# Optimization experiments

Hardware: AMD Instinct MI355X
Metric: run time of the kernel (lower is better)

Reference implementation:

```python
import jax, jax.numpy as jnp
import numpy as np
from jax import lax

MU = 0.1          # cfg MODEL.MU (FISTA step size)
LMBD = 0.1        # cfg MODEL.LAMBDA[0]
N_STEPS = 4       # cfg MODEL.NUM_LAYERS (unrolled FISTA iterations)
BN_EPS = 1e-5


def _norm_w(W):
    # DictBlock w_norm: each dictionary filter normalized to unit L2 norm.
    # torch does this under no_grad (in-place on .data), so the norm is a constant.
    n = jnp.sqrt(jnp.sum(W * W, axis=(1, 2, 3), keepdims=True))
    return W / lax.stop_gradient(n + 1e-12)


def _conv(x, W, stride, pad):
    return lax.conv_general_dilated(x, W, (stride, stride), [(pad, pad)] * 2,
                                    dimension_numbers=('NCHW', 'OIHW', 'NCHW'))


def _conv_t(z, W, stride, pad, out_pad):
    # torch conv_transpose2d(z, W, stride, padding=pad, output_padding=out_pad)
    k = W.shape[2]
    Wt = jnp.transpose(jnp.flip(W, (2, 3)), (1, 0, 2, 3))  # (in_ch, dict, k, k)
    p = k - 1 - pad
    return lax.conv_general_dilated(z, Wt, (1, 1), [(p, p + out_pad)] * 2,
                                    lhs_dilation=(stride, stride),
                                    dimension_numbers=('NCHW', 'OIHW', 'NCHW'))


def _shrink(c):
    # non-negative soft threshold: relu(c - lmbd*step)
    return jax.nn.relu(c - LMBD * MU)


def _dict_conv(x, W, stride):
    # Unrolled FISTA sparse coding: min_c 0.5||x - W^T c||^2 + lmbd||c||_1, c>=0
    W = _norm_w(W)
    out_pad = stride - 1
    c = _shrink(MU * _conv(x, W, stride, 1))
    c_pre = jnp.zeros_like(c)
    t = 1.0
    for _ in range(N_STEPS - 1):
        t_next = (1.0 + float(np.sqrt(1.0 + 4.0 * t * t))) / 2.0
        a = c + ((t - 1.0) / t_next) * (c - c_pre)
        c_pre = c
        r = x - _conv_t(a, W, stride, 1, out_pad)       # reconstruction residual
        c = _shrink(a + MU * _conv(r, W, stride, 1))    # proximal gradient step
        t = t_next
    return c


def _bn(x, g, b, m, v):
    # eval-mode BatchNorm2d with running stats
    scale = g * lax.rsqrt(v + BN_EPS)
    return (x - m[None, :, None, None]) * scale[None, :, None, None] + b[None, :, None, None]


def setup_inputs() -> dict:
    key = jax.random.key(0)
    ks = jax.random.split(key, 12)
    N, Cin, Cout, H = 32, 128, 256, 56
    x = jax.random.normal(ks[0], (N, Cin, H, H), jnp.float32)
    def unit_norm(W):
        return W / (jnp.sqrt(jnp.sum(W * W, axis=(1, 2, 3), keepdims=True)) + 1e-12)
    W1 = unit_norm(jax.random.normal(ks[1], (Cout, Cin, 3, 3), jnp.float32))
    W2 = unit_norm(jax.random.normal(ks[2], (Cout, Cout, 3, 3), jnp.float32))
    Wsc = jax.random.normal(ks[3], (Cout, Cin, 1, 1), jnp.float32) * 0.05
    def bn(k):
        k1, k2, k3, k4 = jax.random.split(k, 4)
        g = 1.0 + 0.1 * jax.random.normal(k1, (Cout,), jnp.float32)
        b = 0.1 * jax.random.normal(k2, (Cout,), jnp.float32)
        m = 0.1 * jax.random.normal(k3, (Cout,), jnp.float32)
        v = 0.5 + jax.random.uniform(k4, (Cout,), jnp.float32)
        return g, b, m, v
    bn1_g, bn1_b, bn1_m, bn1_v = bn(ks[4])
    bn2_g, bn2_b, bn2_m, bn2_v = bn(ks[5])
    bnsc_g, bnsc_b, bnsc_m, bnsc_v = bn(ks[6])
    return dict(x=x, W1=W1, W2=W2, Wsc=Wsc,
                bn1_g=bn1_g, bn1_b=bn1_b, bn1_m=bn1_m, bn1_v=bn1_v,
                bn2_g=bn2_g, bn2_b=bn2_b, bn2_m=bn2_m, bn2_v=bn2_v,
                bnsc_g=bnsc_g, bnsc_b=bnsc_b, bnsc_m=bnsc_m, bnsc_v=bnsc_v)


def reference(x, W1, W2, Wsc,
              bn1_g, bn1_b, bn1_m, bn1_v,
              bn2_g, bn2_b, bn2_m, bn2_v,
              bnsc_g, bnsc_b, bnsc_m, bnsc_v):
    out = _bn(_dict_conv(x, W1, 2), bn1_g, bn1_b, bn1_m, bn1_v)
    out = _bn(_dict_conv(out, W2, 1), bn2_g, bn2_b, bn2_m, bn2_v)
    sc = _bn(_conv(x, Wsc, 2, 0), bnsc_g, bnsc_b, bnsc_m, bnsc_v)
    return jax.nn.relu(out + sc)
```

## Files before the change

kernel.cpp:

```cpp
#include <hip/hip_runtime.h>
#include <math.h>

#define MU_F 0.1f
#define SHRINK_F 0.01f
#define BN_EPS_F 1e-5f

typedef _Float16 half_t;
typedef _Float16 half8 __attribute__((ext_vector_type(8)));
typedef float f32x4 __attribute__((ext_vector_type(4)));

#define LROW 40

template<int KS, int S, int PAD, int MODE>
__global__ __launch_bounds__(256, 2)
void conv_big(const half_t* __restrict__ Ag, const half_t* __restrict__ Xh,
              float* __restrict__ outF, half_t* __restrict__ outH,
              const half_t* __restrict__ auxH, const float* __restrict__ auxF,
              int CA, int Cout, int Hin, int Win, int Hout, int Wout, int ptiles,
              float alpha, float beta, float delta, int relu1,
              const float* __restrict__ pscale, const float* __restrict__ pbias,
              const float* __restrict__ aux3, int relu2)
{
    __shared__ __align__(16) half_t sm[256 * LROW];
    half_t* LA = sm;
    half_t* LB = sm + 128 * LROW;

    const int tid = threadIdx.x;
    const int wv = tid >> 6, ln = tid & 63;
    const int n = blockIdx.z;
    const int co0 = blockIdx.y * 128;
    const int wco = (wv & 1) * 64, wpx = (wv >> 1) * 64;

    int eh = 0, ew = 0, p0;
    if (MODE == 2) {
        int q = blockIdx.x / ptiles;
        p0 = (blockIdx.x - q * ptiles) * 128;
        eh = q >> 1; ew = q & 1;
    } else {
        p0 = blockIdx.x * 128;
    }

    const int Wd  = (MODE == 2) ? (Wout >> 1) : Wout;
    const int Hd  = (MODE == 2) ? (Hout >> 1) : Hout;
    const int PHW = Hd * Wd;
    const int K9  = KS * KS * CA;

    const int part = tid & 3;
    const int row0 = tid >> 2;

    size_t abase[2];
    abase[0] = (size_t)(co0 + row0) * K9 + part * 8;
    abase[1] = abase[0] + (size_t)64 * K9;

    int bph[2], bpw[2];
    bool bok0[2];
#pragma unroll
    for (int i = 0; i < 2; ++i) {
        int px = p0 + row0 + i * 64;
        bok0[i] = px < PHW;
        int ph = bok0[i] ? (px / Wd) : 0;
        bph[i] = ph; bpw[i] = px - ph * Wd;
    }

    f32x4 acc[4][4] = {};

    for (int kh = 0; kh < KS; ++kh)
    for (int kw = 0; kw < KS; ++kw) {
        if (MODE == 2) {
            if ((((kh ^ (eh + 1)) & 1) != 0) || (((kw ^ (ew + 1)) & 1) != 0)) continue;
        }
        const int tap = kh * KS + kw;
        size_t bb[2]; bool bvld[2];
#pragma unroll
        for (int i = 0; i < 2; ++i) {
            bool ok = bok0[i];
            int hh, ww2;
            if (MODE == 0) {
                hh = bph[i] * S - PAD + kh; ww2 = bpw[i] * S - PAD + kw;
                ok = ok && (unsigned)hh < (unsigned)Hin && (unsigned)ww2 < (unsigned)Win;
            } else if (MODE == 1) {
                hh = bph[i] + PAD - kh; ww2 = bpw[i] + PAD - kw;
                ok = ok && (unsigned)hh < (unsigned)Hin && (unsigned)ww2 < (unsigned)Win;
            } else {
                int nh = 2 * bph[i] + eh + PAD - kh, nw = 2 * bpw[i] + ew + PAD - kw;
                hh = nh >> 1; ww2 = nw >> 1;
                ok = ok && nh >= 0 && nw >= 0 && hh < Hin && ww2 < Win;
            }
            bvld[i] = ok;
            bb[i] = ok ? (((size_t)(n * Hin + hh) * Win + ww2) * CA + part * 8) : 0;
        }
        const size_t atap = (size_t)tap * CA;

        for (int c0 = 0; c0 < CA; c0 += 32) {
            half8 a0 = *(const half8*)(Ag + abase[0] + atap + c0);
            half8 a1 = *(const half8*)(Ag + abase[1] + atap + c0);
            half8 b0 = {}, b1 = {};
            if (bvld[0]) b0 = *(const half8*)(Xh + bb[0] + c0);
            if (bvld[1]) b1 = *(const half8*)(Xh + bb[1] + c0);
            *(half8*)(LA +  row0       * LROW + part * 8) = a0;
            *(half8*)(LA + (row0 + 64) * LROW + part * 8) = a1;
            *(half8*)(LB +  row0       * LROW + part * 8) = b0;
            *(half8*)(LB + (row0 + 64) * LROW + part * 8) = b1;
            __syncthreads();

            const int fr = ln & 15;
            const int koh = (ln >> 4) * 8;
            half8 fa[4], fb[4];
#pragma unroll
            for (int m = 0; m < 4; ++m)
                fa[m] = *(const half8*)(LA + (wco + m * 16 + fr) * LROW + koh);
#pragma unroll
            for (int t = 0; t < 4; ++t)
                fb[t] = *(const half8*)(LB + (wpx + t * 16 + fr) * LROW + koh);
#pragma unroll
            for (int m = 0; m < 4; ++m)
#pragma unroll
                for (int t = 0; t < 4; ++t)
                    acc[m][t] = __builtin_amdgcn_mfma_f32_16x16x32_f16(fa[m], fb[t], acc[m][t], 0, 0, 0);
            __syncthreads();
        }
    }

    const int fr = ln & 15;
    const int rg = ln >> 4;
#pragma unroll
    for (int t = 0; t < 4; ++t) {
        int px = p0 + wpx + t * 16 + fr;
        if (px >= PHW) continue;
        int ph = px / Wd, pw = px - ph * Wd;
        int oh, ow;
        if (MODE == 2) { oh = 2 * ph + eh; ow = 2 * pw + ew; }
        else           { oh = ph;          ow = pw; }
        size_t ghwc = ((size_t)(n * Hout + oh) * Wout + ow) * Cout;
#pragma unroll
        for (int m = 0; m < 4; ++m) {
#pragma unroll
            for (int r = 0; r < 4; ++r) {
                int co_l = co0 + wco + m * 16 + rg * 4 + r;
                size_t fidx = ((size_t)(n * Cout + co_l) * Hout + oh) * Wout + ow;
                float v = alpha * acc[m][t][r] + delta;
                if (auxH) v += beta * (float)auxH[ghwc + co_l];
                if (auxF) v += beta * auxF[fidx];
                if (relu1) v = fmaxf(v, 0.f);
                if (pscale) v = pscale[co_l] * v + pbias[co_l];
                if (aux3) v += aux3[fidx];
                if (relu2) v = fmaxf(v, 0.f);
                if (outH) outH[ghwc + co_l] = (half_t)v;
                else      outF[fidx] = v;
            }
        }
    }
}

template<int KT>
__global__ __launch_bounds__(256)
void pack_w(const float* __restrict__ W, half_t* __restrict__ Wh,
            half_t* __restrict__ WTh, int Cin, int Cout, int do_norm)
{
    __shared__ float red[256];
    int co = blockIdx.x, tid = threadIdx.x;
    int CK = Cin * KT;
    const float* w = W + (size_t)co * CK;
    float inv = 1.f;
    if (do_norm) {
        float s = 0.f;
        for (int i = tid; i < CK; i += 256) { float v = w[i]; s += v * v; }
        red[tid] = s; __syncthreads();
        for (int o = 128; o > 0; o >>= 1) {
            if (tid < o) red[tid] += red[tid + o];
            __syncthreads();
        }
        inv = 1.f / (sqrtf(red[0]) + 1e-12f);
    }
    for (int i = tid; i < CK; i += 256) {
        int ci = i / KT, tap = i - ci * KT;
        half_t h = (half_t)(w[i] * inv);
        Wh[((size_t)co * KT + tap) * Cin + ci] = h;
        if (WTh) WTh[((size_t)ci * KT + tap) * Cout + co] = h;
    }
}

__global__ __launch_bounds__(256)
void tx_kernel(const float* __restrict__ x, half_t* __restrict__ xTh)
{
    __shared__ __align__(16) half_t tl[56 * 136];
    int h = blockIdx.x, n = blockIdx.y, tid = threadIdx.x;
    for (int it = 0; it < 28; ++it) {
        int id = tid + it * 256;
        int c = id / 56, w0 = id - c * 56;
        tl[w0 * 136 + c] = (half_t)x[(((size_t)n * 128 + c) * 56 + h) * 56 + w0];
    }
    __syncthreads();
    if (tid < 224) {
        int w0 = tid >> 2, part = tid & 3;
        size_t base = (((size_t)n * 56 + h) * 56 + w0) * 128 + part * 32;
#pragma unroll
        for (int j = 0; j < 4; ++j)
            *(half8*)(xTh + base + j * 8) = *(const half8*)(tl + w0 * 136 + part * 32 + j * 8);
    }
}

__global__ __launch_bounds__(256)
void comb_kernel(const half_t* __restrict__ c, const half_t* __restrict__ p,
                 half_t* __restrict__ a, float w1, float w2, int n8)
{
    int i = blockIdx.x * 256 + threadIdx.x;
    if (i >= n8) return;
    half8 cv = ((const half8*)c)[i];
    half8 pv = ((const half8*)p)[i];
    half8 r;
#pragma unroll
    for (int j = 0; j < 8; ++j) r[j] = (half_t)(w1 * (float)cv[j] + w2 * (float)pv[j]);
    ((half8*)a)[i] = r;
}

__global__ __launch_bounds__(256)
void bn_prep_kernel(const float* __restrict__ g, const float* __restrict__ b,
                    const float* __restrict__ m, const float* __restrict__ v,
                    float* __restrict__ s, float* __restrict__ t, int C)
{
    int i = blockIdx.x * 256 + threadIdx.x;
    if (i < C) {
        float sc = g[i] * rsqrtf(v[i] + BN_EPS_F);
        s[i] = sc; t[i] = b[i] - m[i] * sc;
    }
}

extern "C" void kernel_launch(void* const* d_in, const int* in_sizes, int n_in,
                              void* d_out, int out_size, void* d_ws, size_t ws_size,
                              hipStream_t stream)
{
    (void)in_sizes; (void)n_in; (void)out_size;
    const float* x    = (const float*)d_in[0];
    const float* W1   = (const float*)d_in[1];
    const float* W2   = (const float*)d_in[2];
    const float* Wsc  = (const float*)d_in[3];
    const float* bn1g = (const float*)d_in[4];
    const float* bn1b = (const float*)d_in[5];
    const float* bn1m = (const float*)d_in[6];
    const float* bn1v = (const float*)d_in[7];
    const float* bn2g = (const float*)d_in[8];
    const float* bn2b = (const float*)d_in[9];
    const float* bn2m = (const float*)d_in[10];
    const float* bn2v = (const float*)d_in[11];
    const float* bscg = (const float*)d_in[12];
    const float* bscb = (const float*)d_in[13];
    const float* bscm = (const float*)d_in[14];
    const float* bscv = (const float*)d_in[15];

    const size_t NB = (size_t)32 * 256 * 28 * 28;
    const size_t NX = (size_t)32 * 128 * 56 * 56;

    char* base = (char*)d_ws;
    size_t off = 0;
    auto alloc = [&](size_t nbytes) -> void* {
        void* r = base + off;
        off = (off + nbytes + 255) & ~(size_t)255;
        return r;
    };
    half_t* Wh1  = (half_t*)alloc(294912 * 2);
    half_t* WTh1 = (half_t*)alloc(294912 * 2);
    half_t* Wh2  = (half_t*)alloc(589824 * 2);
    half_t* WTh2 = (half_t*)alloc(589824 * 2);
    half_t* Wsch = (half_t*)alloc(32768 * 2);
    float* bn1s = (float*)alloc(256 * 4);  float* bn1t = (float*)alloc(256 * 4);
    float* bn2s = (float*)alloc(256 * 4);  float* bn2t = (float*)alloc(256 * 4);
    float* bscs = (float*)alloc(256 * 4);  float* bsct = (float*)alloc(256 * 4);
    half_t* xTh  = (half_t*)alloc(NX * 2);
    half_t* r56h = xTh;
    half_t* Pa   = (half_t*)alloc(NB * 2);
    half_t* Pb   = (half_t*)alloc(NB * 2);
    half_t* Pc   = (half_t*)alloc(NB * 2);
    half_t* Py   = (half_t*)alloc(NB * 2);
    half_t* r28h = (half_t*)alloc(NB * 2);
    float*  scF  = (float*)alloc(NB * 4);
    if (off > ws_size) return;

    float* outp = (float*)d_out;

    double t = 1.0; float al[3];
    for (int i = 0; i < 3; ++i) {
        double tn = (1.0 + sqrt(1.0 + 4.0 * t * t)) / 2.0;
        al[i] = (float)((t - 1.0) / tn); t = tn;
    }

    const dim3 blk(256);
    const dim3 gF(7, 2, 32);
    const dim3 gT2(28, 1, 32);
    const int n8 = (int)(NB / 8);
    const dim3 gC((n8 + 255) / 256);
    const float* NF = nullptr;
    const half_t* NH = nullptr;
    float* NFo = nullptr;
    half_t* NHo = nullptr;

    pack_w<9><<<256, blk, 0, stream>>>(W1, Wh1, WTh1, 128, 256, 1);
    pack_w<9><<<256, blk, 0, stream>>>(W2, Wh2, WTh2, 256, 256, 1);
    pack_w<1><<<256, blk, 0, stream>>>(Wsc, Wsch, nullptr, 128, 256, 0);
    bn_prep_kernel<<<1, blk, 0, stream>>>(bn1g, bn1b, bn1m, bn1v, bn1s, bn1t, 256);
    bn_prep_kernel<<<1, blk, 0, stream>>>(bn2g, bn2b, bn2m, bn2v, bn2s, bn2t, 256);
    bn_prep_kernel<<<1, blk, 0, stream>>>(bscg, bscb, bscm, bscv, bscs, bsct, 256);
    tx_kernel<<<dim3(56, 32), blk, 0, stream>>>(x, xTh);

    conv_big<3,2,1,0><<<gF, blk, 0, stream>>>(Wh1, xTh, NFo, Pa, NH, NF,
        128, 256, 56, 56, 28, 28, 7, MU_F, 0.f, -SHRINK_F, 1, NF, NF, NF, 0);
    conv_big<1,2,0,0><<<gF, blk, 0, stream>>>(Wsch, xTh, scF, NHo, NH, NF,
        128, 256, 56, 56, 28, 28, 7, 1.f, 0.f, 0.f, 0, bscs, bsct, NF, 0);

    conv_big<3,2,1,2><<<gT2, blk, 0, stream>>>(WTh1, Pa, NFo, r56h, NH, x,
        256, 128, 28, 28, 56, 56, 7, -1.f, 1.f, 0.f, 0, NF, NF, NF, 0);
    conv_big<3,2,1,0><<<gF, blk, 0, stream>>>(Wh1, r56h, NFo, Pb, Pa, NF,
        128, 256, 56, 56, 28, 28, 7, MU_F, 1.f, -SHRINK_F, 1, NF, NF, NF, 0);

    comb_kernel<<<gC, blk, 0, stream>>>(Pb, Pa, Pc, 1.f + al[1], -al[1], n8);
    conv_big<3,2,1,2><<<gT2, blk, 0, stream>>>(WTh1, Pc, NFo, r56h, NH, x,
        256, 128, 28, 28, 56, 56, 7, -1.f, 1.f, 0.f, 0, NF, NF, NF, 0);
    conv_big<3,2,1,0><<<gF, blk, 0, stream>>>(Wh1, r56h, NFo, Pa, Pc, NF,
        128, 256, 56, 56, 28, 28, 7, MU_F, 1.f, -SHRINK_F, 1, NF, NF, NF, 0);

    comb_kernel<<<gC, blk, 0, stream>>>(Pa, Pb, Pc, 1.f + al[2], -al[2], n8);
    conv_big<3,2,1,2><<<gT2, blk, 0, stream>>>(WTh1, Pc, NFo, r56h, NH, x,
        256, 128, 28, 28, 56, 56, 7, -1.f, 1.f, 0.f, 0, NF, NF, NF, 0);
    conv_big<3,2,1,0><<<gF, blk, 0, stream>>>(Wh1, r56h, NFo, Py, Pc, NF,
        128, 256, 56, 56, 28, 28, 7, MU_F, 1.f, -SHRINK_F, 1, bn1s, bn1t, NF, 0);

    conv_big<3,1,1,0><<<gF, blk, 0, stream>>>(Wh2, Py, NFo, Pa, NH, NF,
        256, 256, 28, 28, 28, 28, 7, MU_F, 0.f, -SHRINK_F, 1, NF, NF, NF, 0);

    conv_big<3,1,1,1><<<gF, blk, 0, stream>>>(WTh2, Pa, NFo, r28h, Py, NF,
        256, 256, 28, 28, 28, 28, 7, -1.f, 1.f, 0.f, 0, NF, NF, NF, 0);
    conv_big<3,1,1,0><<<gF, blk, 0, stream>>>(Wh2, r28h, NFo, Pb, Pa, NF,
        256, 256, 28, 28, 28, 28, 7, MU_F, 1.f, -SHRINK_F, 1, NF, NF, NF, 0);

    comb_kernel<<<gC, blk, 0, stream>>>(Pb, Pa, Pc, 1.f + al[1], -al[1], n8);
    conv_big<3,1,1,1><<<gF, blk, 0, stream>>>(WTh2, Pc, NFo, r28h, Py, NF,
        256, 256, 28, 28, 28, 28, 7, -1.f, 1.f, 0.f, 0, NF, NF, NF, 0);
    conv_big<3,1,1,0><<<gF, blk, 0, stream>>>(Wh2, r28h, NFo, Pa, Pc, NF,
        256, 256, 28, 28, 28, 28, 7, MU_F, 1.f, -SHRINK_F, 1, NF, NF, NF, 0);

    comb_kernel<<<gC, blk, 0, stream>>>(Pa, Pb, Pc, 1.f + al[2], -al[2], n8);
    conv_big<3,1,1,1><<<gF, blk, 0, stream>>>(WTh2, Pc, NFo, r28h, Py, NF,
        256, 256, 28, 28, 28, 28, 7, -1.f, 1.f, 0.f, 0, NF, NF, NF, 0);
    conv_big<3,1,1,0><<<gF, blk, 0, stream>>>(Wh2, r28h, outp, NHo, Pc, NF,
        256, 256, 28, 28, 28, 28, 7, MU_F, 1.f, -SHRINK_F, 1, bn2s, bn2t, scF, 1);
}
```

Baseline: 1.330 ms.

## Double-buffer LDS tiles and prefetch next K-chunk into registers in conv GEMM

Flattens the tap×channel-chunk loops into a single loop and double-buffers the shared-memory tiles, so the global loads for step k+2 are in flight while MFMAs run on step k. This removes one of the two barriers per iteration and hides global-load latency behind compute. In exchange it doubles LDS use (40 KB per block), which may limit occupancy at two blocks per CU, and it assumes CA/32 is 4 or 8 (power-of-two channel-chunk count).

```diff
diff --git a/kernel.cpp b/kernel.cpp
--- a/kernel.cpp
+++ b/kernel.cpp
@@ -21,9 +21,7 @@
               const float* __restrict__ pscale, const float* __restrict__ pbias,
               const float* __restrict__ aux3, int relu2)
 {
-    __shared__ __align__(16) half_t sm[256 * LROW];
-    half_t* LA = sm;
-    half_t* LB = sm + 128 * LROW;
+    __shared__ __align__(16) half_t sm[2 * 256 * LROW];
 
     const int tid = threadIdx.x;
     const int wv = tid >> 6, ln = tid & 63;
@@ -48,12 +46,10 @@
     const int part = tid & 3;
     const int row0 = tid >> 2;
 
-    size_t abase[2];
-    abase[0] = (size_t)(co0 + row0) * K9 + part * 8;
-    abase[1] = abase[0] + (size_t)64 * K9;
-
-    int bph[2], bpw[2];
-    bool bok0[2];
+    const size_t abase0 = (size_t)(co0 + row0) * K9 + part * 8;
+    const size_t abase1 = abase0 + (size_t)64 * K9;
+
+    int bph[2], bpw[2]; bool bok0[2];
 #pragma unroll
     for (int i = 0; i < 2; ++i) {
         int px = p0 + row0 + i * 64;
@@ -62,19 +58,35 @@
         bph[i] = ph; bpw[i] = px - ph * Wd;
     }
 
-    f32x4 acc[4][4] = {};
-
-    for (int kh = 0; kh < KS; ++kh)
-    for (int kw = 0; kw < KS; ++kw) {
+    const int cpt = CA >> 5;
+    const int lgc = (cpt == 8) ? 3 : 2;
+    int ntap, lgj = 0, phh = 0, pww = 0;
+    if (MODE == 2) {
+        phh = (eh + 1) & 1; pww = (ew + 1) & 1;
+        lgj = ew;
+        ntap = (1 + eh) * (1 + ew);
+    } else {
+        ntap = KS * KS;
+    }
+    const int total = ntap << lgc;
+
+    auto fetch = [&](int flat, half8& a0, half8& a1, half8& b0, half8& b1) {
+        const int ci = flat & (cpt - 1);
+        const int ti = flat >> lgc;
+        int kh, kw;
         if (MODE == 2) {
-            if ((((kh ^ (eh + 1)) & 1) != 0) || (((kw ^ (ew + 1)) & 1) != 0)) continue;
-        }
-        const int tap = kh * KS + kw;
-        size_t bb[2]; bool bvld[2];
+            int i2 = ti >> lgj, j = ti & ((1 << lgj) - 1);
+            kh = phh + 2 * i2; kw = pww + 2 * j;
+        } else if (KS == 3) {
+            kh = (ti * 11) >> 5; kw = ti - 3 * kh;
+        } else { kh = 0; kw = 0; }
+        const int c0 = ci << 5;
+        const size_t aoff = (size_t)(kh * KS + kw) * CA + c0;
+        a0 = *(const half8*)(Ag + abase0 + aoff);
+        a1 = *(const half8*)(Ag + abase1 + aoff);
 #pragma unroll
         for (int i = 0; i < 2; ++i) {
-            bool ok = bok0[i];
-            int hh, ww2;
+            bool ok = bok0[i]; int hh, ww2;
             if (MODE == 0) {
                 hh = bph[i] * S - PAD + kh; ww2 = bpw[i] * S - PAD + kw;
                 ok = ok && (unsigned)hh < (unsigned)Hin && (unsigned)ww2 < (unsigned)Win;
@@ -86,42 +98,52 @@
                 hh = nh >> 1; ww2 = nw >> 1;
                 ok = ok && nh >= 0 && nw >= 0 && hh < Hin && ww2 < Win;
             }
-            bvld[i] = ok;
-            bb[i] = ok ? (((size_t)(n * Hin + hh) * Win + ww2) * CA + part * 8) : 0;
+            half8 v = {};
+            if (ok) v = *(const half8*)(Xh + ((size_t)(n * Hin + hh) * Win + ww2) * CA + c0 + part * 8);
+            if (i == 0) b0 = v; else b1 = v;
         }
-        const size_t atap = (size_t)tap * CA;
-
-        for (int c0 = 0; c0 < CA; c0 += 32) {
-            half8 a0 = *(const half8*)(Ag + abase[0] + atap + c0);
-            half8 a1 = *(const half8*)(Ag + abase[1] + atap + c0);
-            half8 b0 = {}, b1 = {};
-            if (bvld[0]) b0 = *(const half8*)(Xh + bb[0] + c0);
-            if (bvld[1]) b1 = *(const half8*)(Xh + bb[1] + c0);
-            *(half8*)(LA +  row0       * LROW + part * 8) = a0;
-            *(half8*)(LA + (row0 + 64) * LROW + part * 8) = a1;
-            *(half8*)(LB +  row0       * LROW + part * 8) = b0;
-            *(half8*)(LB + (row0 + 64) * LROW + part * 8) = b1;
-            __syncthreads();
-
-            const int fr = ln & 15;
-            const int koh = (ln >> 4) * 8;
-            half8 fa[4], fb[4];
-#pragma unroll
-            for (int m = 0; m < 4; ++m)
-                fa[m] = *(const half8*)(LA + (wco + m * 16 + fr) * LROW + koh);
-#pragma unroll
-            for (int t = 0; t < 4; ++t)
-                fb[t] = *(const half8*)(LB + (wpx + t * 16 + fr) * LROW + koh);
-#pragma unroll
-            for (int m = 0; m < 4; ++m)
-#pragma unroll
-                for (int t = 0; t < 4; ++t)
-                    acc[m][t] = __builtin_amdgcn_mfma_f32_16x16x32_f16(fa[m], fb[t], acc[m][t], 0, 0, 0);
+    };
+
+    f32x4 acc[4][4] = {};
+    half8 pa0, pa1, pb0, pb1;
+
+    fetch(0, pa0, pa1, pb0, pb1);
+    {
+        half_t* buf = sm;
+        *(half8*)(buf +  row0        * LROW + part * 8) = pa0;
+        *(half8*)(buf + (row0 +  64) * LROW + part * 8) = pa1;
+        *(half8*)(buf + (row0 + 128) * LROW + part * 8) = pb0;
+        *(half8*)(buf + (row0 + 192) * LROW + part * 8) = pb1;
+    }
+    if (total > 1) fetch(1, pa0, pa1, pb0, pb1);
+    __syncthreads();
+
+    const int fr = ln & 15, koh = (ln >> 4) * 8;
+    for (int k = 0; k < total; ++k) {
+        half_t* buf = sm + (k & 1) * (256 * LROW);
+        half8 fa[4], fb[4];
+#pragma unroll
+        for (int m = 0; m < 4; ++m)
+            fa[m] = *(const half8*)(buf + (wco + m * 16 + fr) * LROW + koh);
+#pragma unroll
+        for (int t2 = 0; t2 < 4; ++t2)
+            fb[t2] = *(const half8*)(buf + (128 + wpx + t2 * 16 + fr) * LROW + koh);
+#pragma unroll
+        for (int m = 0; m < 4; ++m)
+#pragma unroll
+            for (int t2 = 0; t2 < 4; ++t2)
+                acc[m][t2] = __builtin_amdgcn_mfma_f32_16x16x32_f16(fa[m], fb[t2], acc[m][t2], 0, 0, 0);
+        if (k + 1 < total) {
+            half_t* nb = sm + ((k + 1) & 1) * (256 * LROW);
+            *(half8*)(nb +  row0        * LROW + part * 8) = pa0;
+            *(half8*)(nb + (row0 +  64) * LROW + part * 8) = pa1;
+            *(half8*)(nb + (row0 + 128) * LROW + part * 8) = pb0;
+            *(half8*)(nb + (row0 + 192) * LROW + part * 8) = pb1;
+            if (k + 2 < total) fetch(k + 2, pa0, pa1, pb0, pb1);
             __syncthreads();
         }
     }
 
-    const int fr = ln & 15;
     const int rg = ln >> 4;
 #pragma unroll
     for (int t = 0; t < 4; ++t) {
```

Result: faster. 1.196 ms (-10.1%).

## Replace LDS-staged conv GEMM with register-direct MFMA fragment loads

Applied to the files above, without the earlier changes.

Drops LDS staging and barriers from the implicit-GEMM convolution. Weights are pre-packed into an MFMA-fragment layout, and each wave loads its A and B fragments straight from global memory into registers. Pixel tiles now span the batch dimension to cover 25088 positions, out-of-bounds taps read a zeroed page instead of branching, and epilogue loads and stores are vectorized. Residuals now go to their own buffer, and the shortcut is stored as fp16 rather than fp32. The trade is losing data reuse across waves through shared memory, so more global and L2 traffic, plus unrolled loops that may raise register pressure.

```diff
diff --git a/kernel.cpp b/kernel.cpp
--- a/kernel.cpp
+++ b/kernel.cpp
@@ -7,146 +7,133 @@
 
 typedef _Float16 half_t;
 typedef _Float16 half8 __attribute__((ext_vector_type(8)));
+typedef _Float16 half4 __attribute__((ext_vector_type(4)));
 typedef float f32x4 __attribute__((ext_vector_type(4)));
 
-#define LROW 40
-
-template<int KS, int S, int PAD, int MODE>
-__global__ __launch_bounds__(256, 2)
-void conv_big(const half_t* __restrict__ Ag, const half_t* __restrict__ Xh,
+template<int KS, int S, int PAD, int MODE, int CAT>
+__global__ __launch_bounds__(256)
+void conv_reg(const half_t* __restrict__ Af, const half_t* __restrict__ Xh,
               float* __restrict__ outF, half_t* __restrict__ outH,
-              const half_t* __restrict__ auxH, const float* __restrict__ auxF,
-              int CA, int Cout, int Hin, int Win, int Hout, int Wout, int ptiles,
-              float alpha, float beta, float delta, int relu1,
+              const half_t* __restrict__ auxH, const half_t* __restrict__ aux3H,
               const float* __restrict__ pscale, const float* __restrict__ pbias,
-              const float* __restrict__ aux3, int relu2)
-{
-    __shared__ __align__(16) half_t sm[256 * LROW];
-    half_t* LA = sm;
-    half_t* LB = sm + 128 * LROW;
-
+              const half_t* __restrict__ zpage,
+              int Cout, int Hin, int Win, int Hout, int Wout, int KT, int ptiles,
+              float alpha, float beta, float delta, int relu1, int relu2)
+{
     const int tid = threadIdx.x;
     const int wv = tid >> 6, ln = tid & 63;
-    const int n = blockIdx.z;
-    const int co0 = blockIdx.y * 128;
-    const int wco = (wv & 1) * 64, wpx = (wv >> 1) * 64;
-
-    int eh = 0, ew = 0, p0;
-    if (MODE == 2) {
-        int q = blockIdx.x / ptiles;
-        p0 = (blockIdx.x - q * ptiles) * 128;
-        eh = q >> 1; ew = q & 1;
-    } else {
-        p0 = blockIdx.x * 128;
-    }
-
-    const int Wd  = (MODE == 2) ? (Wout >> 1) : Wout;
-    const int Hd  = (MODE == 2) ? (Hout >> 1) : Hout;
-    const int PHW = Hd * Wd;
-    const int K9  = KS * KS * CA;
-
-    const int part = tid & 3;
-    const int row0 = tid >> 2;
-
-    size_t abase[2];
-    abase[0] = (size_t)(co0 + row0) * K9 + part * 8;
-    abase[1] = abase[0] + (size_t)64 * K9;
-
-    int bph[2], bpw[2];
-    bool bok0[2];
-#pragma unroll
-    for (int i = 0; i < 2; ++i) {
-        int px = p0 + row0 + i * 64;
-        bok0[i] = px < PHW;
-        int ph = bok0[i] ? (px / Wd) : 0;
-        bph[i] = ph; bpw[i] = px - ph * Wd;
-    }
-
+    const int g  = blockIdx.y * 2 + (wv & 1);
+    const int fr = ln & 15, rg = ln >> 4, ko8 = rg * 8;
+    const int PXTOT = 25088;
+
+    int eh = 0, ew = 0, bx = blockIdx.x;
+    if (MODE == 2) { int q = bx / ptiles; bx -= q * ptiles; eh = q >> 1; ew = q & 1; }
+    const int p0 = bx * 128 + (wv >> 1) * 64;
+
+    const int Wd   = (MODE == 2) ? (Wout >> 1) : Wout;
+    const int Hd   = (MODE == 2) ? (Hout >> 1) : Hout;
+    const int PHWI = Hd * Wd;
+
+    int phv[4], pwv[4], nv[4];
+    unsigned vb[4];
+#pragma unroll
+    for (int t = 0; t < 4; ++t) {
+        int px = p0 + t * 16 + fr;
+        int n  = px / PHWI; int rem = px - n * PHWI;
+        int ph = rem / Wd;  int pw  = rem - ph * Wd;
+        nv[t] = n; phv[t] = ph; pwv[t] = pw;
+        int ih0 = (MODE == 0) ? ph * S : ph;
+        int iw0 = (MODE == 0) ? pw * S : pw;
+        vb[t] = ((unsigned)(n * Hin + ih0) * Win + iw0) * CAT + ko8;
+    }
+
+    const half_t* Ap = Af + ((size_t)g * KT) * 2048 + ln * 8;
     f32x4 acc[4][4] = {};
-
+    constexpr int cpt = CAT / 32;
+
+#pragma unroll
     for (int kh = 0; kh < KS; ++kh)
+#pragma unroll
     for (int kw = 0; kw < KS; ++kw) {
-        if (MODE == 2) {
+        int dh, dw;
+        if (MODE == 0)      { dh = kh - PAD; dw = kw - PAD; }
+        else if (MODE == 1) { dh = PAD - kh; dw = PAD - kw; }
+        else {
             if ((((kh ^ (eh + 1)) & 1) != 0) || (((kw ^ (ew + 1)) & 1) != 0)) continue;
+            dh = (eh + PAD - kh) >> 1; dw = (ew + PAD - kw) >> 1;
+        }
+        const int off = (dh * Win + dw) * CAT;
+        const half_t* bp[4];
+#pragma unroll
+        for (int t = 0; t < 4; ++t) {
+            int ih = ((MODE == 0) ? phv[t] * S : phv[t]) + dh;
+            int iw = ((MODE == 0) ? pwv[t] * S : pwv[t]) + dw;
+            bool ok = (unsigned)ih < (unsigned)Hin && (unsigned)iw < (unsigned)Win;
+            bp[t] = ok ? (Xh + vb[t] + off) : zpage;
         }
         const int tap = kh * KS + kw;
-        size_t bb[2]; bool bvld[2];
-#pragma unroll
-        for (int i = 0; i < 2; ++i) {
-            bool ok = bok0[i];
-            int hh, ww2;
-            if (MODE == 0) {
-                hh = bph[i] * S - PAD + kh; ww2 = bpw[i] * S - PAD + kw;
-                ok = ok && (unsigned)hh < (unsigned)Hin && (unsigned)ww2 < (unsigned)Win;
-            } else if (MODE == 1) {
-                hh = bph[i] + PAD - kh; ww2 = bpw[i] + PAD - kw;
-                ok = ok && (unsigned)hh < (unsigned)Hin && (unsigned)ww2 < (unsigned)Win;
-            } else {
-                int nh = 2 * bph[i] + eh + PAD - kh, nw = 2 * bpw[i] + ew + PAD - kw;
-                hh = nh >> 1; ww2 = nw >> 1;
-                ok = ok && nh >= 0 && nw >= 0 && hh < Hin && ww2 < Win;
-            }
-            bvld[i] = ok;
-            bb[i] = ok ? (((size_t)(n * Hin + hh) * Win + ww2) * CA + part * 8) : 0;
-        }
-        const size_t atap = (size_t)tap * CA;
-
-        for (int c0 = 0; c0 < CA; c0 += 32) {
-            half8 a0 = *(const half8*)(Ag + abase[0] + atap + c0);
-            half8 a1 = *(const half8*)(Ag + abase[1] + atap + c0);
-            half8 b0 = {}, b1 = {};
-            if (bvld[0]) b0 = *(const half8*)(Xh + bb[0] + c0);
-            if (bvld[1]) b1 = *(const half8*)(Xh + bb[1] + c0);
-            *(half8*)(LA +  row0       * LROW + part * 8) = a0;
-            *(half8*)(LA + (row0 + 64) * LROW + part * 8) = a1;
-            *(half8*)(LB +  row0       * LROW + part * 8) = b0;
-            *(half8*)(LB + (row0 + 64) * LROW + part * 8) = b1;
-            __syncthreads();
-
-            const int fr = ln & 15;
-            const int koh = (ln >> 4) * 8;
+        const half_t* Apt = Ap + (size_t)(tap * cpt) * 2048;
+#pragma unroll
+        for (int ci = 0; ci < cpt; ++ci) {
             half8 fa[4], fb[4];
 #pragma unroll
             for (int m = 0; m < 4; ++m)
-                fa[m] = *(const half8*)(LA + (wco + m * 16 + fr) * LROW + koh);
+                fa[m] = *(const half8*)(Apt + ci * 2048 + m * 512);
 #pragma unroll
             for (int t = 0; t < 4; ++t)
-                fb[t] = *(const half8*)(LB + (wpx + t * 16 + fr) * LROW + koh);
+                fb[t] = *(const half8*)(bp[t] + ci * 32);
 #pragma unroll
             for (int m = 0; m < 4; ++m)
 #pragma unroll
                 for (int t = 0; t < 4; ++t)
                     acc[m][t] = __builtin_amdgcn_mfma_f32_16x16x32_f16(fa[m], fb[t], acc[m][t], 0, 0, 0);
-            __syncthreads();
-        }
-    }
-
-    const int fr = ln & 15;
-    const int rg = ln >> 4;
+        }
+    }
+
 #pragma unroll
     for (int t = 0; t < 4; ++t) {
-        int px = p0 + wpx + t * 16 + fr;
-        if (px >= PHW) continue;
-        int ph = px / Wd, pw = px - ph * Wd;
         int oh, ow;
-        if (MODE == 2) { oh = 2 * ph + eh; ow = 2 * pw + ew; }
-        else           { oh = ph;          ow = pw; }
-        size_t ghwc = ((size_t)(n * Hout + oh) * Wout + ow) * Cout;
+        if (MODE == 2) { oh = 2 * phv[t] + eh; ow = 2 * pwv[t] + ew; }
+        else           { oh = phv[t];          ow = pwv[t]; }
+        size_t gb = ((size_t)(nv[t] * Hout + oh) * Wout + ow) * Cout + g * 64;
 #pragma unroll
         for (int m = 0; m < 4; ++m) {
-#pragma unroll
-            for (int r = 0; r < 4; ++r) {
-                int co_l = co0 + wco + m * 16 + rg * 4 + r;
-                size_t fidx = ((size_t)(n * Cout + co_l) * Hout + oh) * Wout + ow;
-                float v = alpha * acc[m][t][r] + delta;
-                if (auxH) v += beta * (float)auxH[ghwc + co_l];
-                if (auxF) v += beta * auxF[fidx];
-                if (relu1) v = fmaxf(v, 0.f);
-                if (pscale) v = pscale[co_l] * v + pbias[co_l];
-                if (aux3) v += aux3[fidx];
-                if (relu2) v = fmaxf(v, 0.f);
-                if (outH) outH[ghwc + co_l] = (half_t)v;
-                else      outF[fidx] = v;
+            const int cb = m * 16 + rg * 4;
+            float v[4];
+#pragma unroll
+            for (int r = 0; r < 4; ++r) v[r] = alpha * acc[m][t][r] + delta;
+            if (auxH) {
+                half4 a1 = *(const half4*)(auxH + gb + cb);
+#pragma unroll
+                for (int r = 0; r < 4; ++r) v[r] += beta * (float)a1[r];
+            }
+            if (relu1)
+#pragma unroll
+                for (int r = 0; r < 4; ++r) v[r] = fmaxf(v[r], 0.f);
+            if (pscale) {
+                f32x4 s = *(const f32x4*)(pscale + g * 64 + cb);
+                f32x4 b = *(const f32x4*)(pbias  + g * 64 + cb);
+#pragma unroll
+                for (int r = 0; r < 4; ++r) v[r] = s[r] * v[r] + b[r];
+            }
+            if (aux3H) {
+                half4 a3 = *(const half4*)(aux3H + gb + cb);
+#pragma unroll
+                for (int r = 0; r < 4; ++r) v[r] += (float)a3[r];
+            }
+            if (relu2)
+#pragma unroll
+                for (int r = 0; r < 4; ++r) v[r] = fmaxf(v[r], 0.f);
+            if (outH) {
+                half4 o;
+#pragma unroll
+                for (int r = 0; r < 4; ++r) o[r] = (half_t)v[r];
+                *(half4*)(outH + gb + cb) = o;
+            } else {
+                const int co = g * 64 + cb;
+#pragma unroll
+                for (int r = 0; r < 4; ++r)
+                    outF[((size_t)(nv[t] * Cout + co + r) * Hout + oh) * Wout + ow] = v[r];
             }
         }
     }
@@ -181,6 +168,20 @@
 }
 
 __global__ __launch_bounds__(256)
+void pack_frag(const half_t* __restrict__ Wflat, half_t* __restrict__ Af,
+               int KT, int total8)
+{
+    int idx = blockIdx.x * 256 + threadIdx.x;
+    if (idx >= total8) return;
+    int l = idx & 63, m = (idx >> 6) & 3, t2 = idx >> 8;
+    int kc = t2 % KT, gg = t2 / KT;
+    int row = gg * 64 + m * 16 + (l & 15);
+    int koff = kc * 32 + (l >> 4) * 8;
+    int K9 = KT * 32;
+    *(half8*)(Af + (size_t)idx * 8) = *(const half8*)(Wflat + (size_t)row * K9 + koff);
+}
+
+__global__ __launch_bounds__(256)
 void tx_kernel(const float* __restrict__ x, half_t* __restrict__ xTh)
 {
     __shared__ __align__(16) half_t tl[56 * 136];
@@ -224,6 +225,13 @@
         float sc = g[i] * rsqrtf(v[i] + BN_EPS_F);
         s[i] = sc; t[i] = b[i] - m[i] * sc;
     }
+}
+
+__global__ __launch_bounds__(256)
+void zero_kernel(half_t* __restrict__ p, int n)
+{
+    int i = blockIdx.x * 256 + threadIdx.x;
+    if (i < n) p[i] = (half_t)0.f;
 }
 
 extern "C" void kernel_launch(void* const* d_in, const int* in_sizes, int n_in,
@@ -263,17 +271,23 @@
     half_t* Wh2  = (half_t*)alloc(589824 * 2);
     half_t* WTh2 = (half_t*)alloc(589824 * 2);
     half_t* Wsch = (half_t*)alloc(32768 * 2);
+    half_t* Af1  = (half_t*)alloc(294912 * 2);
+    half_t* AfT1 = (half_t*)alloc(294912 * 2);
+    half_t* Af2  = (half_t*)alloc(589824 * 2);
+    half_t* AfT2 = (half_t*)alloc(589824 * 2);
+    half_t* Afsc = (half_t*)alloc(32768 * 2);
     float* bn1s = (float*)alloc(256 * 4);  float* bn1t = (float*)alloc(256 * 4);
     float* bn2s = (float*)alloc(256 * 4);  float* bn2t = (float*)alloc(256 * 4);
     float* bscs = (float*)alloc(256 * 4);  float* bsct = (float*)alloc(256 * 4);
+    half_t* zp   = (half_t*)alloc(512 * 2);
     half_t* xTh  = (half_t*)alloc(NX * 2);
-    half_t* r56h = xTh;
+    half_t* r56h = (half_t*)alloc(NX * 2);
     half_t* Pa   = (half_t*)alloc(NB * 2);
     half_t* Pb   = (half_t*)alloc(NB * 2);
     half_t* Pc   = (half_t*)alloc(NB * 2);
     half_t* Py   = (half_t*)alloc(NB * 2);
     half_t* r28h = (half_t*)alloc(NB * 2);
-    float*  scF  = (float*)alloc(NB * 4);
+    half_t* Psc  = (half_t*)alloc(NB * 2);
     if (off > ws_size) return;
 
     float* outp = (float*)d_out;
@@ -285,8 +299,8 @@
     }
 
     const dim3 blk(256);
-    const dim3 gF(7, 2, 32);
-    const dim3 gT2(28, 1, 32);
+    const dim3 gF(196, 2);
+    const dim3 gT2(784, 1);
     const int n8 = (int)(NB / 8);
     const dim3 gC((n8 + 255) / 256);
     const float* NF = nullptr;
@@ -297,50 +311,56 @@
     pack_w<9><<<256, blk, 0, stream>>>(W1, Wh1, WTh1, 128, 256, 1);
     pack_w<9><<<256, blk, 0, stream>>>(W2, Wh2, WTh2, 256, 256, 1);
     pack_w<1><<<256, blk, 0, stream>>>(Wsc, Wsch, nullptr, 128, 256, 0);
+    pack_frag<<<(36864 + 255) / 256, blk, 0, stream>>>(Wh1,  Af1,  36, 36864);
+    pack_frag<<<(36864 + 255) / 256, blk, 0, stream>>>(WTh1, AfT1, 72, 36864);
+    pack_frag<<<(73728 + 255) / 256, blk, 0, stream>>>(Wh2,  Af2,  72, 73728);
+    pack_frag<<<(73728 + 255) / 256, blk, 0, stream>>>(WTh2, AfT2, 72, 73728);
+    pack_frag<<<(4096  + 255) / 256, blk, 0, stream>>>(Wsch, Afsc,  4, 4096);
     bn_prep_kernel<<<1, blk, 0, stream>>>(bn1g, bn1b, bn1m, bn1v, bn1s, bn1t, 256);
     bn_prep_kernel<<<1, blk, 0, stream>>>(bn2g, bn2b, bn2m, bn2v, bn2s, bn2t, 256);
     bn_prep_kernel<<<1, blk, 0, stream>>>(bscg, bscb, bscm, bscv, bscs, bsct, 256);
+    zero_kernel<<<2, blk, 0, stream>>>(zp, 512);
     tx_kernel<<<dim3(56, 32), blk, 0, stream>>>(x, xTh);
 
-    conv_big<3,2,1,0><<<gF, blk, 0, stream>>>(Wh1, xTh, NFo, Pa, NH, NF,
-        128, 256, 56, 56, 28, 28, 7, MU_F, 0.f, -SHRINK_F, 1, NF, NF, NF, 0);
-    conv_big<1,2,0,0><<<gF, blk, 0, stream>>>(Wsch, xTh, scF, NHo, NH, NF,
-        128, 256, 56, 56, 28, 28, 7, 1.f, 0.f, 0.f, 0, bscs, bsct, NF, 0);
-
-    conv_big<3,2,1,2><<<gT2, blk, 0, stream>>>(WTh1, Pa, NFo, r56h, NH, x,
-        256, 128, 28, 28, 56, 56, 7, -1.f, 1.f, 0.f, 0, NF, NF, NF, 0);
-    conv_big<3,2,1,0><<<gF, blk, 0, stream>>>(Wh1, r56h, NFo, Pb, Pa, NF,
-        128, 256, 56, 56, 28, 28, 7, MU_F, 1.f, -SHRINK_F, 1, NF, NF, NF, 0);
+    conv_reg<3,2,1,0,128><<<gF, blk, 0, stream>>>(Af1, xTh, NFo, Pa, NH, NH, NF, NF, zp,
+        256, 56, 56, 28, 28, 36, 196, MU_F, 0.f, -SHRINK_F, 1, 0);
+    conv_reg<1,2,0,0,128><<<gF, blk, 0, stream>>>(Afsc, xTh, NFo, Psc, NH, NH, bscs, bsct, zp,
+        256, 56, 56, 28, 28, 4, 196, 1.f, 0.f, 0.f, 0, 0);
+
+    conv_reg<3,2,1,2,256><<<gT2, blk, 0, stream>>>(AfT1, Pa, NFo, r56h, xTh, NH, NF, NF, zp,
+        128, 28, 28, 56, 56, 72, 196, -1.f, 1.f, 0.f, 0, 0);
+    conv_reg<3,2,1,0,128><<<gF, blk, 0, stream>>>(Af1, r56h, NFo, Pb, Pa, NH, NF, NF, zp,
+        256, 56, 56, 28, 28, 36, 196, MU_F, 1.f, -SHRINK_F, 1, 0);
 
     comb_kernel<<<gC, blk, 0, stream>>>(Pb, Pa, Pc, 1.f + al[1], -al[1], n8);
-    conv_big<3,2,1,2><<<gT2, blk, 0, stream>>>(WTh1, Pc, NFo, r56h, NH, x,
-        256, 128, 28, 28, 56, 56, 7, -1.f, 1.f, 0.f, 0, NF, NF, NF, 0);
-    conv_big<3,2,1,0><<<gF, blk, 0, stream>>>(Wh1, r56h, NFo, Pa, Pc, NF,
-        128, 256, 56, 56, 28, 28, 7, MU_F, 1.f, -SHRINK_F, 1, NF, NF, NF, 0);
+    conv_reg<3,2,1,2,256><<<gT2, blk, 0, stream>>>(AfT1, Pc, NFo, r56h, xTh, NH, NF, NF, zp,
+        128, 28, 28, 56, 56, 72, 196, -1.f, 1.f, 0.f, 0, 0);
+    conv_reg<3,2,1,0,128><<<gF, blk, 0, stream>>>(Af1, r56h, NFo, Pa, Pc, NH, NF, NF, zp,
+        256, 56, 56, 28, 28, 36, 196, MU_F, 1.f, -SHRINK_F, 1, 0);
 
     comb_kernel<<<gC, blk, 0, stream>>>(Pa, Pb, Pc, 1.f + al[2], -al[2], n8);
-    conv_big<3,2,1,2><<<gT2, blk, 0, stream>>>(WTh1, Pc, NFo, r56h, NH, x,
-        256, 128, 28, 28, 56, 56, 7, -1.f, 1.f, 0.f, 0, NF, NF, NF, 0);
-    conv_big<3,2,1,0><<<gF, blk, 0, stream>>>(Wh1, r56h, NFo, Py, Pc, NF,
-        128, 256, 56, 56, 28, 28, 7, MU_F, 1.f, -SHRINK_F, 1, bn1s, bn1t, NF, 0);
-
-    conv_big<3,1,1,0><<<gF, blk, 0, stream>>>(Wh2, Py, NFo, Pa, NH, NF,
-        256, 256, 28, 28, 28, 28, 7, MU_F, 0.f, -SHRINK_F, 1, NF, NF, NF, 0);
-
-    conv_big<3,1,1,1><<<gF, blk, 0, stream>>>(WTh2, Pa, NFo, r28h, Py, NF,
-        256, 256, 28, 28, 28, 28, 7, -1.f, 1.f, 0.f, 0, NF, NF, NF, 0);
-    conv_big<3,1,1,0><<<gF, blk, 0, stream>>>(Wh2, r28h, NFo, Pb, Pa, NF,
-        256, 256, 28, 28, 28, 28, 7, MU_F, 1.f, -SHRINK_F, 1, NF, NF, NF, 0);
+    conv_reg<3,2,1,2,256><<<gT2, blk, 0, stream>>>(AfT1, Pc, NFo, r56h, xTh, NH, NF, NF, zp,
+        128, 28, 28, 56, 56, 72, 196, -1.f, 1.f, 0.f, 0, 0);
+    conv_reg<3,2,1,0,128><<<gF, blk, 0, stream>>>(Af1, r56h, NFo, Py, Pc, NH, bn1s, bn1t, zp,
+        256, 56, 56, 28, 28, 36, 196, MU_F, 1.f, -SHRINK_F, 1, 0);
+
+    conv_reg<3,1,1,0,256><<<gF, blk, 0, stream>>>(Af2, Py, NFo, Pa, NH, NH, NF, NF, zp,
+        256, 28, 28, 28, 28, 72, 196, MU_F, 0.f, -SHRINK_F, 1, 0);
+
+    conv_reg<3,1,1,1,256><<<gF, blk, 0, stream>>>(AfT2, Pa, NFo, r28h, Py, NH, NF, NF, zp,
+        256, 28, 28, 28, 28, 72, 196, -1.f, 1.f, 0.f, 0, 0);
+    conv_reg<3,1,1,0,256><<<gF, blk, 0, stream>>>(Af2, r28h, NFo, Pb, Pa, NH, NF, NF, zp,
+        256, 28, 28, 28, 28, 72, 196, MU_F, 1.f, -SHRINK_F, 1, 0);
 
     comb_kernel<<<gC, blk, 0, stream>>>(Pb, Pa, Pc, 1.f + al[1], -al[1], n8);
-    conv_big<3,1,1,1><<<gF, blk, 0, stream>>>(WTh2, Pc, NFo, r28h, Py, NF,
-        256, 256, 28, 28, 28, 28, 7, -1.f, 1.f, 0.f, 0, NF, NF, NF, 0);
-    conv_big<3,1,1,0><<<gF, blk, 0, stream>>>(Wh2, r28h, NFo, Pa, Pc, NF,
-        256, 256, 28, 28, 28, 28, 7, MU_F, 1.f, -SHRINK_F, 1, NF, NF, NF, 0);
+    conv_reg<3,1,1,1,256><<<gF, blk, 0, stream>>>(AfT2, Pc, NFo, r28h, Py, NH, NF, NF, zp,
+        256, 28, 28, 28, 28, 72, 196, -1.f, 1.f, 0.f, 0, 0);
+    conv_reg<3,1,1,0,256><<<gF, blk, 0, stream>>>(Af2, r28h, NFo, Pa, Pc, NH, NF, NF, zp,
+        256, 28, 28, 28, 28, 72, 196, MU_F, 1.f, -SHRINK_F, 1, 0);
 
     comb_kernel<<<gC, blk, 0, stream>>>(Pa, Pb, Pc, 1.f + al[2], -al[2], n8);
-    conv_big<3,1,1,1><<<gF, blk, 0, stream>>>(WTh2, Pc, NFo, r28h, Py, NF,
-        256, 256, 28, 28, 28, 28, 7, -1.f, 1.f, 0.f, 0, NF, NF, NF, 0);
-    conv_big<3,1,1,0><<<gF, blk, 0, stream>>>(Wh2, r28h, outp, NHo, Pc, NF,
-        256, 256, 28, 28, 28, 28, 7, MU_F, 1.f, -SHRINK_F, 1, bn2s, bn2t, scF, 1);
-}
+    conv_reg<3,1,1,1,256><<<gF, blk, 0, stream>>>(AfT2, Pc, NFo, r28h, Py, NH, NF, NF, zp,
+        256, 28, 28, 28, 28, 72, 196, -1.f, 1.f, 0.f, 0, 0);
+    conv_reg<3,1,1,0,256><<<gF, blk, 0, stream>>>(Af2, r28h, outp, NHo, Pc, Psc, bn2s, bn2t, zp,
+        256, 28, 28, 28, 28, 72, 196, MU_F, 1.f, -SHRINK_F, 1, 1);
+}
```

Result: no change. 1.315 ms (-1.1%).
